# Optimization experiments

Hardware: AMD Instinct MI355X
Metric: run time of the kernel (lower is better)

The kernel has to match this reference:

```python
import jax, jax.numpy as jnp
import numpy as np


def setup_inputs() -> dict:
    key = jax.random.key(0)
    k1, k2 = jax.random.split(key)
    b, c, n = 16, 64, 65536
    features = jax.random.normal(k1, (b, c, n), dtype=jnp.float32)
    coords = jax.random.normal(k2, (b, 3, n), dtype=jnp.float32)  # roughly in [-1,1], clamp handles outliers
    return {"features": features, "coords": coords, "resolution": 32}


def reference(features, coords, resolution):
    r = int(resolution)
    r2, r3 = r * r, r * r * r
    b, c, n = features.shape
    # scale_pvcnn path: map coords from [-1,1] to voxel space, clamp, round
    norm_coords = jnp.clip(((coords + 1.0) / 2.0) * r, 0.0, r - 1)
    vox_coords = jnp.round(norm_coords).astype(jnp.int32)
    # linear voxel index per point: [b, n]
    indices = vox_coords[:, 0] * r2 + vox_coords[:, 1] * r + vox_coords[:, 2]
    # append ones channel for counting
    feat1 = jnp.concatenate(
        [features, jnp.ones((b, 1, n), dtype=features.dtype)], axis=1
    )  # [b, c+1, n]

    def scatter_one(f, idx):  # f: [c+1, n], idx: [n]
        return jnp.zeros((c + 1, r3), dtype=f.dtype).at[:, idx].add(f)

    out = jax.vmap(scatter_one)(feat1, indices)  # [b, c+1, r^3]
    cnt = out[:, -1:, :]
    cnt = jnp.where(cnt == 0, jnp.asarray(1e-5, cnt.dtype), cnt)
    vox_feature = (out[:, :-1, :] / cnt).reshape(b, c, r, r, r)
    return vox_feature, norm_coords
```

## Files before the change

kernel.cpp:

```cpp
#include <hip/hip_runtime.h>

constexpr int Rr = 32;
constexpr int R2 = Rr * Rr;
constexpr int R3 = Rr * Rr * Rr;
constexpr int Bb = 16;
constexpr int Cc = 64;
constexpr int Nn = 65536;
constexpr int VOX_ELEMS = Bb * Cc * R3;
constexpr int NCELL = Bb * R3;

__device__ __forceinline__ unsigned pack_bf16(float a, float b)
{
    unsigned ua = __float_as_uint(a);
    unsigned ub = __float_as_uint(b);
    ua += 0x7FFFu + ((ua >> 16) & 1u);
    ub += 0x7FFFu + ((ub >> 16) & 1u);
    return (ua >> 16) | (ub & 0xFFFF0000u);
}

__global__ __launch_bounds__(256) void vox_coords_kernel(
    const float* __restrict__ coords,
    float* __restrict__ norm_out,
    int* __restrict__ idx_out,
    int* __restrict__ cnt)
{
    int t = blockIdx.x * 256 + threadIdx.x;
    int b = t >> 16;
    int i = t & (Nn - 1);

    const float* cp = coords + (size_t)b * 3 * Nn + i;
    float x = cp[0];
    float y = cp[Nn];
    float z = cp[2 * Nn];

    float nx = fminf(fmaxf((x + 1.0f) * 16.0f, 0.0f), 31.0f);
    float ny = fminf(fmaxf((y + 1.0f) * 16.0f, 0.0f), 31.0f);
    float nz = fminf(fmaxf((z + 1.0f) * 16.0f, 0.0f), 31.0f);

    float* np_ = norm_out + (size_t)b * 3 * Nn + i;
    np_[0]      = nx;
    np_[Nn]     = ny;
    np_[2 * Nn] = nz;

    int idx = (int)rintf(nx) * R2 + (int)rintf(ny) * Rr + (int)rintf(nz);

    idx_out[t] = idx;
    atomicAdd(&cnt[(b << 15) + idx], 1);
}

__global__ __launch_bounds__(256) void inv_kernel(
    const int* __restrict__ cnt, float* __restrict__ inv)
{
    int t = blockIdx.x * 256 + threadIdx.x;
    int c = cnt[t];
    inv[t] = c ? 1.0f / (float)c : 0.0f;
}

__global__ __launch_bounds__(256) void tscatter_atomic_kernel(
    const float* __restrict__ feat,
    const int* __restrict__ idx_ws,
    const float* __restrict__ inv,
    unsigned short* __restrict__ voxT)
{
    __shared__ float lds[64 * 65];
    __shared__ int   cell_sm[64];
    __shared__ float inv_sm[64];
    int b    = blockIdx.x >> 10;
    int tile = blockIdx.x & 1023;
    int n0   = tile << 6;
    int t    = threadIdx.x;

    if (t < 64) {
        int cell = (b << 15) + idx_ws[(b << 16) + n0 + t];
        cell_sm[t] = cell;
        inv_sm[t]  = inv[cell];
    }

#pragma unroll
    for (int k = 0; k < 4; ++k) {
        int c  = (t >> 4) + (k << 4);
        int n4 = (t & 15) << 2;
        float4 v = *(const float4*)(feat + (((size_t)(b * Cc + c)) << 16) + n0 + n4);
        lds[(n4 + 0) * 65 + c] = v.x;
        lds[(n4 + 1) * 65 + c] = v.y;
        lds[(n4 + 2) * 65 + c] = v.z;
        lds[(n4 + 3) * 65 + c] = v.w;
    }
    __syncthreads();

    int wave = t >> 6, lane = t & 63;
    int hi = lane >> 5;
    int m  = lane & 31;
#pragma unroll
    for (int k = 0; k < 8; ++k) {
        int n = (wave << 4) + (k << 1) + hi;
        float s  = inv_sm[n];
        float f0 = lds[n * 65 + (m << 1) + 0] * s;
        float f1 = lds[n * 65 + (m << 1) + 1] * s;
        unsigned pk = pack_bf16(f0, f1);
        unsigned short* addr = voxT + ((size_t)cell_sm[n] << 6) + (m << 1);
        asm volatile("global_atomic_pk_add_bf16 %0, %1, off"
                     :: "v"(addr), "v"(pk) : "memory");
    }
}

__global__ __launch_bounds__(256) void transpose_out_kernel(
    const unsigned short* __restrict__ voxT, float* __restrict__ vox)
{
    __shared__ float lds[64 * 65];
    int b    = blockIdx.x >> 9;
    int tile = blockIdx.x & 511;
    int v0   = tile << 6;
    int t    = threadIdx.x;

#pragma unroll
    for (int k = 0; k < 4; ++k) {
        int v  = (t >> 4) + (k << 4);
        int c4 = (t & 15) << 2;
        ushort4 w = *(const ushort4*)(voxT + (((size_t)(b << 15) + v0 + v) << 6) + c4);
        lds[v * 65 + c4 + 0] = __uint_as_float((unsigned)w.x << 16);
        lds[v * 65 + c4 + 1] = __uint_as_float((unsigned)w.y << 16);
        lds[v * 65 + c4 + 2] = __uint_as_float((unsigned)w.z << 16);
        lds[v * 65 + c4 + 3] = __uint_as_float((unsigned)w.w << 16);
    }
    __syncthreads();

    int wave = t >> 6, lane = t & 63;
#pragma unroll
    for (int k = 0; k < 16; ++k) {
        int c = (wave << 4) + k;
        vox[(((size_t)(b * Cc + c)) << 15) + v0 + lane] = lds[lane * 65 + c];
    }
}

extern "C" void kernel_launch(void* const* d_in, const int* in_sizes, int n_in,
                              void* d_out, int out_size, void* d_ws, size_t ws_size,
                              hipStream_t stream)
{
    const float* features = (const float*)d_in[0];
    const float* coords   = (const float*)d_in[1];

    float* out      = (float*)d_out;
    float* vox      = out;
    float* norm_out = out + VOX_ELEMS;

    char* ws = (char*)d_ws;
    int*            cnt    = (int*)ws;            ws += (size_t)NCELL * 4;
    float*          inv    = (float*)ws;          ws += (size_t)NCELL * 4;
    int*            idx_ws = (int*)ws;            ws += (size_t)Bb * Nn * 4;
    unsigned short* voxT   = (unsigned short*)ws;

    hipMemsetAsync(cnt, 0, (size_t)NCELL * sizeof(int), stream);
    hipMemsetAsync(voxT, 0, (size_t)NCELL * 64 * sizeof(unsigned short), stream);

    vox_coords_kernel<<<(Bb * Nn) / 256, 256, 0, stream>>>(coords, norm_out, idx_ws, cnt);
    inv_kernel<<<NCELL / 256, 256, 0, stream>>>(cnt, inv);
    tscatter_atomic_kernel<<<Bb * 1024, 256, 0, stream>>>(features, idx_ws, inv, voxT);
    transpose_out_kernel<<<Bb * 512, 256, 0, stream>>>(voxT, vox);
}
```

Before: 259.8 us.

## Replace bf16 atomic scatter with per-point slot stores and merge pass

Each point now claims a rank within its voxel from the count atomic and packs it into the index word. Up to three points per voxel write plain stores into private slots, and further points accumulate atomically into a fourth slot that is zeroed only where needed. A merge kernel sums the slots, divides by the count, and transposes to the output. This drops the full voxT memset, the inv kernel and most bf16 atomics, at the cost of a four-times larger intermediate buffer and extra reads in the merge.

After: 224.7 us, median of 2. -13.5%, faster.

```diff
diff --git a/kernel.cpp b/kernel.cpp
--- a/kernel.cpp
+++ b/kernel.cpp
@@ -16,6 +16,12 @@
     ua += 0x7FFFu + ((ua >> 16) & 1u);
     ub += 0x7FFFu + ((ub >> 16) & 1u);
     return (ua >> 16) | (ub & 0xFFFF0000u);
+}
+
+__global__ __launch_bounds__(256) void zero_cnt_kernel(float4* __restrict__ base)
+{
+    int i = blockIdx.x * 256 + threadIdx.x;
+    base[i] = float4{0.0f, 0.0f, 0.0f, 0.0f};
 }
 
 __global__ __launch_bounds__(256) void vox_coords_kernel(
@@ -44,41 +50,47 @@
 
     int idx = (int)rintf(nx) * R2 + (int)rintf(ny) * Rr + (int)rintf(nz);
 
-    idx_out[t] = idx;
-    atomicAdd(&cnt[(b << 15) + idx], 1);
+    int k = atomicAdd(&cnt[(b << 15) + idx], 1);
+    idx_out[t] = (idx << 3) | min(k, 7);
 }
 
-__global__ __launch_bounds__(256) void inv_kernel(
-    const int* __restrict__ cnt, float* __restrict__ inv)
+__global__ __launch_bounds__(256) void slot3zero_kernel(
+    const int* __restrict__ cnt, unsigned short* __restrict__ voxT4)
 {
-    int t = blockIdx.x * 256 + threadIdx.x;
-    int c = cnt[t];
-    inv[t] = c ? 1.0f / (float)c : 0.0f;
+    int g = blockIdx.x * 256 + threadIdx.x;
+    int cell = g >> 3;
+    int p    = g & 7;
+    if (cnt[cell] > 4)
+        *(float4*)(voxT4 + ((size_t)cell << 8) + 192 + (p << 3)) =
+            float4{0.0f, 0.0f, 0.0f, 0.0f};
 }
 
-__global__ __launch_bounds__(256) void tscatter_atomic_kernel(
+__global__ __launch_bounds__(256) void tscatter_store_kernel(
     const float* __restrict__ feat,
     const int* __restrict__ idx_ws,
-    const float* __restrict__ inv,
-    unsigned short* __restrict__ voxT)
+    const int* __restrict__ cnt,
+    unsigned short* __restrict__ voxT4)
 {
     __shared__ float lds[64 * 65];
-    __shared__ int   cell_sm[64];
-    __shared__ float inv_sm[64];
+    __shared__ int   dest_sm[64];
+    __shared__ int   at_sm[64];
     int b    = blockIdx.x >> 10;
     int tile = blockIdx.x & 1023;
     int n0   = tile << 6;
     int t    = threadIdx.x;
 
     if (t < 64) {
-        int cell = (b << 15) + idx_ws[(b << 16) + n0 + t];
-        cell_sm[t] = cell;
-        inv_sm[t]  = inv[cell];
+        int e    = idx_ws[(b << 16) + n0 + t];
+        int cell = (b << 15) + (e >> 3);
+        int k    = e & 7;
+        int cn   = cnt[cell];
+        dest_sm[t] = (cell << 8) + (min(k, 3) << 6);
+        at_sm[t]   = (k >= 3 && cn > 4) ? 1 : 0;
     }
 
 #pragma unroll
-    for (int k = 0; k < 4; ++k) {
-        int c  = (t >> 4) + (k << 4);
+    for (int q = 0; q < 4; ++q) {
+        int c  = (t >> 4) + (q << 4);
         int n4 = (t & 15) << 2;
         float4 v = *(const float4*)(feat + (((size_t)(b * Cc + c)) << 16) + n0 + n4);
         lds[(n4 + 0) * 65 + c] = v.x;
@@ -92,37 +104,64 @@
     int hi = lane >> 5;
     int m  = lane & 31;
 #pragma unroll
-    for (int k = 0; k < 8; ++k) {
-        int n = (wave << 4) + (k << 1) + hi;
-        float s  = inv_sm[n];
-        float f0 = lds[n * 65 + (m << 1) + 0] * s;
-        float f1 = lds[n * 65 + (m << 1) + 1] * s;
+    for (int kk = 0; kk < 8; ++kk) {
+        int n = (wave << 4) + (kk << 1) + hi;
+        float f0 = lds[n * 65 + (m << 1) + 0];
+        float f1 = lds[n * 65 + (m << 1) + 1];
         unsigned pk = pack_bf16(f0, f1);
-        unsigned short* addr = voxT + ((size_t)cell_sm[n] << 6) + (m << 1);
-        asm volatile("global_atomic_pk_add_bf16 %0, %1, off"
-                     :: "v"(addr), "v"(pk) : "memory");
+        unsigned short* addr = voxT4 + (size_t)dest_sm[n] + (m << 1);
+        if (at_sm[n]) {
+            asm volatile("global_atomic_pk_add_bf16 %0, %1, off"
+                         :: "v"(addr), "v"(pk) : "memory");
+        } else {
+            *(unsigned*)addr = pk;
+        }
     }
 }
 
-__global__ __launch_bounds__(256) void transpose_out_kernel(
-    const unsigned short* __restrict__ voxT, float* __restrict__ vox)
+__global__ __launch_bounds__(256) void merge_transpose_kernel(
+    const unsigned short* __restrict__ voxT4,
+    const int* __restrict__ cnt,
+    float* __restrict__ vox)
 {
     __shared__ float lds[64 * 65];
     int b    = blockIdx.x >> 9;
     int tile = blockIdx.x & 511;
     int v0   = tile << 6;
     int t    = threadIdx.x;
+    int cl   = t >> 2;
+    int q    = t & 3;
 
+    int cell = (b << 15) + v0 + cl;
+    int cn   = cnt[cell];
+    int kmax = min(cn, 4);
+
+    float acc[16];
 #pragma unroll
-    for (int k = 0; k < 4; ++k) {
-        int v  = (t >> 4) + (k << 4);
-        int c4 = (t & 15) << 2;
-        ushort4 w = *(const ushort4*)(voxT + (((size_t)(b << 15) + v0 + v) << 6) + c4);
-        lds[v * 65 + c4 + 0] = __uint_as_float((unsigned)w.x << 16);
-        lds[v * 65 + c4 + 1] = __uint_as_float((unsigned)w.y << 16);
-        lds[v * 65 + c4 + 2] = __uint_as_float((unsigned)w.z << 16);
-        lds[v * 65 + c4 + 3] = __uint_as_float((unsigned)w.w << 16);
+    for (int j = 0; j < 16; ++j) acc[j] = 0.0f;
+
+    const unsigned short* base = voxT4 + ((size_t)cell << 8) + (q << 4);
+    for (int k = 0; k < kmax; ++k) {
+        uint4 w0 = *(const uint4*)(base + (k << 6));
+        uint4 w1 = *(const uint4*)(base + (k << 6) + 8);
+        const unsigned* w = &w0.x;
+#pragma unroll
+        for (int j = 0; j < 4; ++j) {
+            acc[2 * j + 0] += __uint_as_float(w[j] << 16);
+            acc[2 * j + 1] += __uint_as_float(w[j] & 0xFFFF0000u);
+        }
+        const unsigned* w2 = &w1.x;
+#pragma unroll
+        for (int j = 0; j < 4; ++j) {
+            acc[8 + 2 * j + 0] += __uint_as_float(w2[j] << 16);
+            acc[8 + 2 * j + 1] += __uint_as_float(w2[j] & 0xFFFF0000u);
+        }
     }
+
+    float inv = cn ? 1.0f / (float)cn : 0.0f;
+#pragma unroll
+    for (int j = 0; j < 16; ++j)
+        lds[cl * 65 + (q << 4) + j] = acc[j] * inv;
     __syncthreads();
 
     int wave = t >> 6, lane = t & 63;
@@ -146,15 +185,12 @@
 
     char* ws = (char*)d_ws;
     int*            cnt    = (int*)ws;            ws += (size_t)NCELL * 4;
-    float*          inv    = (float*)ws;          ws += (size_t)NCELL * 4;
     int*            idx_ws = (int*)ws;            ws += (size_t)Bb * Nn * 4;
-    unsigned short* voxT   = (unsigned short*)ws;
+    unsigned short* voxT4  = (unsigned short*)ws;
 
-    hipMemsetAsync(cnt, 0, (size_t)NCELL * sizeof(int), stream);
-    hipMemsetAsync(voxT, 0, (size_t)NCELL * 64 * sizeof(unsigned short), stream);
-
+    zero_cnt_kernel<<<NCELL * 4 / 16 / 256, 256, 0, stream>>>((float4*)cnt);
     vox_coords_kernel<<<(Bb * Nn) / 256, 256, 0, stream>>>(coords, norm_out, idx_ws, cnt);
-    inv_kernel<<<NCELL / 256, 256, 0, stream>>>(cnt, inv);
-    tscatter_atomic_kernel<<<Bb * 1024, 256, 0, stream>>>(features, idx_ws, inv, voxT);
-    transpose_out_kernel<<<Bb * 512, 256, 0, stream>>>(voxT, vox);
+    slot3zero_kernel<<<NCELL * 8 / 256, 256, 0, stream>>>(cnt, voxT4);
+    tscatter_store_kernel<<<Bb * 1024, 256, 0, stream>>>(features, idx_ws, cnt, voxT4);
+    merge_transpose_kernel<<<Bb * 512, 256, 0, stream>>>(voxT4, cnt, vox);
 }
```
